# Kernel tuning notes

Measured on AMD Instinct MI355X. Metric: run time of the kernel, lower is better.

Reference implementation:

```python
import jax, jax.numpy as jnp
import numpy as np

N_NODES = 50000
N_EDGES = 1600000
N_FEAT = 128
DROPOUT = 0.1


def setup_inputs() -> dict:
    key = jax.random.key(0)
    k1, k2, k3, k4 = jax.random.split(key, 4)
    x = jax.random.normal(k1, (N_NODES, N_FEAT), dtype=jnp.float32)
    adj_vals = jax.random.uniform(k2, (N_EDGES,), dtype=jnp.float32)
    row = jax.random.randint(k3, (N_EDGES,), 0, N_NODES, dtype=jnp.int32)
    col = jax.random.randint(k4, (N_EDGES,), 0, N_NODES, dtype=jnp.int32)
    return {"x": x, "adj_vals": adj_vals, "row": row, "col": col}


def reference(x, adj_vals, row, col):
    # MixedDropout on sparse adjacency values (deterministic fixed key),
    # then SpMM: out[i] = sum_{e: row[e]==i} A_drop[e] * x[col[e]]
    keep_prob = 1.0 - DROPOUT
    mask_key = jax.random.fold_in(jax.random.key(42), 7)
    keep = jax.random.bernoulli(mask_key, keep_prob, adj_vals.shape)
    vals_drop = jnp.where(keep, adj_vals / keep_prob, 0.0)
    # gather source features and weight by (dropped) edge values
    msgs = vals_drop[:, None] * x[col]  # [E, F]
    out = jax.ops.segment_sum(msgs, row, num_segments=N_NODES)  # [N, F]
    return out
```

## Files before the change

### kernel.cpp

```cpp
#include <hip/hip_runtime.h>
#include <stdint.h>

#define N_NODES 50000
#define N_EDGES 1600000
#define N_FEAT 128
#define CAP 64
#define OVF_PW 256
#define OVF_PB 192

#define RSHIFT 8
#define BROWS 256
#define NB 196
#define NWG_A 250
#define A_THREADS 1024
#define CHUNKS_PW 1600
#define CAPW 56
#define NREG (NWG_A + NB)


struct KeyPair { uint32_t a, b; };

__host__ __device__ constexpr inline uint32_t rotl32(uint32_t x, int r) {
  return (x << r) | (x >> (32 - r));
}

__host__ __device__ constexpr inline KeyPair threefry2x32(uint32_t k0, uint32_t k1,
                                                          uint32_t x0, uint32_t x1) {
  const uint32_t ks0 = k0, ks1 = k1, ks2 = k0 ^ k1 ^ 0x1BD11BDAu;
  x0 += ks0;
  x1 += ks1;
  const int rotA[4] = {13, 15, 26, 6};
  const int rotB[4] = {17, 29, 16, 24};
  const uint32_t ks[3] = {ks0, ks1, ks2};
  for (int i = 0; i < 5; ++i) {
    const int* rot = (i & 1) ? rotB : rotA;
    for (int j = 0; j < 4; ++j) {
      x0 += x1;
      x1 = rotl32(x1, rot[j]);
      x1 ^= x0;
    }
    x0 += ks[(i + 1) % 3];
    x1 += ks[(i + 2) % 3] + (uint32_t)(i + 1);
  }
  return {x0, x1};
}

constexpr KeyPair MASK_KEY = threefry2x32(0u, 42u, 0u, 7u);

__device__ inline bool edge_keep(uint32_t e) {
  KeyPair r = threefry2x32(MASK_KEY.a, MASK_KEY.b, 0u, e);
  uint32_t bits = r.a ^ r.b;
  float u = __uint_as_float((bits >> 9) | 0x3f800000u) - 1.0f;
  return u < 0.9f;
}

__device__ inline uint32_t f2bf(uint32_t b) {
  return (b + 0x7fffu + ((b >> 16) & 1u)) >> 16;
}

typedef uint32_t u4v __attribute__((ext_vector_type(4)));
typedef float f4v __attribute__((ext_vector_type(4)));


__global__ void __launch_bounds__(A_THREADS) convA_kernel(const float* __restrict__ x,
                                                          uint32_t* __restrict__ xb,
                                                          const float* __restrict__ adj_vals,
                                                          const int* __restrict__ row,
                                                          const int* __restrict__ col,
                                                          uint64_t* __restrict__ coarse,
                                                          uint32_t* __restrict__ lens,
                                                          uint32_t* __restrict__ ovfcA,
                                                          uint64_t* __restrict__ ovfA) {
  __shared__ uint32_t cnt[NB];
  __shared__ uint32_t ovfc;
  int wg = blockIdx.x;
  int tid = threadIdx.x;
  if (tid < NB) cnt[tid] = 0;
  if (tid == 0) ovfc = 0;

  const int gthreads = NWG_A * A_THREADS;
  for (int i = wg * A_THREADS + tid; i < (N_NODES * N_FEAT) / 8; i += gthreads) {
    f4v a = ((const f4v*)x)[2 * i];
    f4v b = ((const f4v*)x)[2 * i + 1];
    u4v o;
    o.x = f2bf(__float_as_uint(a.x)) | (f2bf(__float_as_uint(a.y)) << 16);
    o.y = f2bf(__float_as_uint(a.z)) | (f2bf(__float_as_uint(a.w)) << 16);
    o.z = f2bf(__float_as_uint(b.x)) | (f2bf(__float_as_uint(b.y)) << 16);
    o.w = f2bf(__float_as_uint(b.z)) | (f2bf(__float_as_uint(b.w)) << 16);
    ((u4v*)xb)[i] = o;
  }
  __syncthreads();

  uint64_t* my_coarse = coarse + (size_t)wg * NB * CAPW;
  for (int ch = tid; ch < CHUNKS_PW; ch += A_THREADS) {
    const int g = wg * CHUNKS_PW + ch;
    const int4 r4 = ((const int4*)row)[g];
    const int4 c4 = ((const int4*)col)[g];
    const float4 a4 = ((const float4*)adj_vals)[g];
    const int rr[4] = {r4.x, r4.y, r4.z, r4.w};
    const int cc[4] = {c4.x, c4.y, c4.z, c4.w};
    const float aa[4] = {a4.x, a4.y, a4.z, a4.w};
#pragma unroll
    for (int k = 0; k < 4; ++k) {
      const uint32_t e = (uint32_t)(4 * g + k);
      if (!edge_keep(e)) continue;
      const uint32_t r = (uint32_t)rr[k];
      const uint32_t c = (uint32_t)cc[k];
      const float v = aa[k] / 0.9f;
      const uint32_t b = r >> RSHIFT;
      const uint32_t li = atomicAdd(&cnt[b], 1u);
      const uint64_t p = ((uint64_t)r << 48) | ((uint64_t)c << 32) | (uint64_t)__float_as_uint(v);
      if (li < CAPW) {
        my_coarse[(size_t)b * CAPW + li] = p;
      } else {
        const uint32_t oi = atomicAdd(&ovfc, 1u);
        if (oi < OVF_PW) ovfA[(size_t)wg * OVF_PW + oi] = p;
      }
    }
  }
  __syncthreads();
  if (tid < NB) lens[(size_t)tid * NWG_A + wg] = min(cnt[tid], (uint32_t)CAPW);
  if (tid == 0) ovfcA[wg] = min(ovfc, (uint32_t)OVF_PW);
}

__global__ void __launch_bounds__(1024) partB_kernel(const uint64_t* __restrict__ coarse,
                                                     const uint32_t* __restrict__ lens,
                                                     uint32_t* __restrict__ payload,
                                                     uint32_t* __restrict__ cursor,
                                                     uint32_t* __restrict__ ovfcB,
                                                     uint64_t* __restrict__ ovfB) {
  int b = blockIdx.x;
  int tid = threadIdx.x;
  __shared__ uint32_t cnt[BROWS];
  __shared__ uint32_t s_len[NWG_A];
  __shared__ uint32_t ovfc;
  if (tid < BROWS) cnt[tid] = 0;
  if (tid < NWG_A) s_len[tid] = lens[(size_t)b * NWG_A + tid];
  if (tid == 0) ovfc = 0;
  __syncthreads();

  int hw = tid >> 5;
  int lane = tid & 31;
  for (int seg = hw; seg < NWG_A; seg += 32) {
    uint32_t len = s_len[seg];
    const uint64_t* cseg = coarse + ((size_t)seg * NB + b) * CAPW;
    for (uint32_t li = (uint32_t)lane; li < len; li += 32) {
      uint64_t p = cseg[li];
      uint32_t r = (uint32_t)(p >> 48);
      uint32_t rl = r & (BROWS - 1);
      uint32_t idx = atomicAdd(&cnt[rl], 1u);
      if (idx < CAP) {
        uint32_t c = (uint32_t)(p >> 32) & 0xFFFFu;
        payload[(size_t)r * CAP + idx] = (c << 16) | f2bf((uint32_t)p);
      } else {
        uint32_t oi = atomicAdd(&ovfc, 1u);
        if (oi < OVF_PB) ovfB[(size_t)b * OVF_PB + oi] = p;
      }
    }
  }
  __syncthreads();
  if (tid < BROWS) {
    uint32_t r = ((uint32_t)b << RSHIFT) + (uint32_t)tid;
    if (r < N_NODES) {
      uint32_t c0 = min(cnt[tid], (uint32_t)CAP);
      cursor[r] = c0;
      uint32_t np = min((c0 + 7u) & ~7u, (uint32_t)CAP);
      for (uint32_t i2 = c0; i2 < np; ++i2) payload[(size_t)r * CAP + i2] = 0u;
    }
  }
  if (tid == 0) ovfcB[b] = min(ovfc, (uint32_t)OVF_PB);
}

__global__ void __launch_bounds__(256) gather_bf16_kernel(const uint32_t* __restrict__ xb,
                                                          const uint32_t* __restrict__ payload,
                                                          const uint32_t* __restrict__ cursor,
                                                          float* __restrict__ out) {
  int r = blockIdx.x * 16 + (threadIdx.x >> 4);
  int lane = threadIdx.x & 15;
  uint32_t base = (uint32_t)r * CAP;
  uint32_t cnt = cursor[r];
  uint32_t n = (cnt + 7u) & ~7u;
  const uint4* x4 = (const uint4*)xb;

  float acc0 = 0.f, acc1 = 0.f, acc2 = 0.f, acc3 = 0.f;
  float acc4 = 0.f, acc5 = 0.f, acc6 = 0.f, acc7 = 0.f;

  uint32_t p0 = __builtin_nontemporal_load(payload + base + lane);
  uint32_t p1 = __builtin_nontemporal_load(payload + base + 16 + lane);
  uint32_t p2 = (n > 32u) ? __builtin_nontemporal_load(payload + base + 32 + lane) : 0u;
  uint32_t p3 = (n > 48u) ? __builtin_nontemporal_load(payload + base + 48 + lane) : 0u;

#define GSTEP(ww)                                                            \
  {                                                                          \
    uint32_t cc = (ww) >> 16;                                                \
    float vv = __uint_as_float((ww) << 16);                                  \
    uint4 a = x4[(size_t)cc * 16 + lane];                                    \
    acc0 += vv * __uint_as_float(a.x << 16);                                 \
    acc1 += vv * __uint_as_float(a.x & 0xffff0000u);                         \
    acc2 += vv * __uint_as_float(a.y << 16);                                 \
    acc3 += vv * __uint_as_float(a.y & 0xffff0000u);                         \
    acc4 += vv * __uint_as_float(a.z << 16);                                 \
    acc5 += vv * __uint_as_float(a.z & 0xffff0000u);                         \
    acc6 += vv * __uint_as_float(a.w << 16);                                 \
    acc7 += vv * __uint_as_float(a.w & 0xffff0000u);                         \
  }

#define PCHUNK(preg, mm)                                                     \
  for (int j = 0; j < (mm); j += 8) {                                        \
    uint32_t w0 = __shfl((preg), j + 0, 16);                                 \
    uint32_t w1 = __shfl((preg), j + 1, 16);                                 \
    uint32_t w2 = __shfl((preg), j + 2, 16);                                 \
    uint32_t w3 = __shfl((preg), j + 3, 16);                                 \
    uint32_t w4 = __shfl((preg), j + 4, 16);                                 \
    uint32_t w5 = __shfl((preg), j + 5, 16);                                 \
    uint32_t w6 = __shfl((preg), j + 6, 16);                                 \
    uint32_t w7 = __shfl((preg), j + 7, 16);                                 \
    GSTEP(w0) GSTEP(w1) GSTEP(w2) GSTEP(w3)                                  \
    GSTEP(w4) GSTEP(w5) GSTEP(w6) GSTEP(w7)                                  \
  }

  int rem = (int)n;
  PCHUNK(p0, min(rem, 16));
  rem -= 16;
  if (rem > 0) {
    PCHUNK(p1, min(rem, 16));
    rem -= 16;
    if (rem > 0) {
      PCHUNK(p2, min(rem, 16));
      rem -= 16;
      if (rem > 0) {
        PCHUNK(p3, min(rem, 16));
      }
    }
  }
#undef PCHUNK
#undef GSTEP

  f4v lo, hi;
  lo.x = acc0; lo.y = acc1; lo.z = acc2; lo.w = acc3;
  hi.x = acc4; hi.y = acc5; hi.z = acc6; hi.w = acc7;
  f4v* o = (f4v*)out + (size_t)r * 32 + lane * 2;
  __builtin_nontemporal_store(lo, o);
  __builtin_nontemporal_store(hi, o + 1);
}

__global__ void __launch_bounds__(256) ovf_pack_kernel(const float* __restrict__ x,
                                                       const uint32_t* __restrict__ ovfcA,
                                                       const uint64_t* __restrict__ ovfA,
                                                       const uint32_t* __restrict__ ovfcB,
                                                       const uint64_t* __restrict__ ovfB,
                                                       float* __restrict__ out) {
  __shared__ int any;
  if (threadIdx.x == 0) any = 0;
  __syncthreads();
  for (int t = threadIdx.x; t < NREG; t += 256) {
    uint32_t c = (t < NWG_A) ? ovfcA[t] : ovfcB[t - NWG_A];
    if (c) any = 1;
  }
  __syncthreads();
  if (!any) return;

  int group = (int)((blockIdx.x * 256 + threadIdx.x) >> 7);
  int f = threadIdx.x & 127;
  const int ngroups = (16 * 256) >> 7;
  for (int reg = group; reg < NREG; reg += ngroups) {
    uint32_t c;
    const uint64_t* basep;
    if (reg < NWG_A) {
      c = min(ovfcA[reg], (uint32_t)OVF_PW);
      basep = ovfA + (size_t)reg * OVF_PW;
    } else {
      c = min(ovfcB[reg - NWG_A], (uint32_t)OVF_PB);
      basep = ovfB + (size_t)(reg - NWG_A) * OVF_PB;
    }
    for (uint32_t i = 0; i < c; ++i) {
      uint64_t p = basep[i];
      uint32_t r = (uint32_t)(p >> 48);
      uint32_t cc = (uint32_t)((p >> 32) & 0xFFFFu);
      float v = __uint_as_float((uint32_t)p);
      atomicAdd(&out[(size_t)r * N_FEAT + f], v * x[(size_t)cc * N_FEAT + f]);
    }
  }
}


__global__ void __launch_bounds__(256) scatter_fused_kernel(const float* __restrict__ x,
                                                            const float* __restrict__ adj_vals,
                                                            const int* __restrict__ row,
                                                            const int* __restrict__ col,
                                                            float* __restrict__ out) {
  long long t = (long long)blockIdx.x * blockDim.x + threadIdx.x;
  int e = (int)(t >> 6);
  int lane = (int)(t & 63);
  if (e >= N_EDGES) return;
  if (!edge_keep((uint32_t)e)) return;
  float v = adj_vals[e] / 0.9f;
  float2 xf = *(const float2*)(x + (long long)col[e] * N_FEAT + lane * 2);
  float* dst = out + (long long)row[e] * N_FEAT + lane * 2;
  atomicAdd(dst, v * xf.x);
  atomicAdd(dst + 1, v * xf.y);
}


extern "C" void kernel_launch(void* const* d_in, const int* in_sizes, int n_in,
                              void* d_out, int out_size, void* d_ws, size_t ws_size,
                              hipStream_t stream) {
  const float* x        = (const float*)d_in[0];
  const float* adj_vals = (const float*)d_in[1];
  const int*   row      = (const int*)d_in[2];
  const int*   col      = (const int*)d_in[3];
  float* out = (float*)d_out;

  size_t a_cursor  = 0;
  size_t a_ovfcA   = (a_cursor + (size_t)N_NODES * 4 + 255) & ~255ull;
  size_t a_ovfcB   = (a_ovfcA + (size_t)NWG_A * 4 + 255) & ~255ull;
  size_t a_lens    = (a_ovfcB + (size_t)NB * 4 + 255) & ~255ull;
  size_t a_ovfA    = (a_lens + (size_t)NB * NWG_A * 4 + 255) & ~255ull;
  size_t a_ovfB    = (a_ovfA + (size_t)NWG_A * OVF_PW * 8 + 255) & ~255ull;
  size_t a_coarse  = (a_ovfB + (size_t)NB * OVF_PB * 8 + 255) & ~255ull;
  size_t a_payload = (a_coarse + (size_t)NWG_A * NB * CAPW * 8 + 255) & ~255ull;
  size_t a_xb      = (a_payload + (size_t)N_NODES * CAP * 4 + 255) & ~255ull;
  size_t need      = a_xb + (size_t)N_NODES * N_FEAT * 2;

  if (ws_size >= need) {
    uint32_t* cursor  = (uint32_t*)((char*)d_ws + a_cursor);
    uint32_t* ovfcA   = (uint32_t*)((char*)d_ws + a_ovfcA);
    uint32_t* ovfcB   = (uint32_t*)((char*)d_ws + a_ovfcB);
    uint32_t* lens    = (uint32_t*)((char*)d_ws + a_lens);
    uint64_t* ovfA    = (uint64_t*)((char*)d_ws + a_ovfA);
    uint64_t* ovfB    = (uint64_t*)((char*)d_ws + a_ovfB);
    uint64_t* coarse  = (uint64_t*)((char*)d_ws + a_coarse);
    uint32_t* payload = (uint32_t*)((char*)d_ws + a_payload);
    uint32_t* xb      = (uint32_t*)((char*)d_ws + a_xb);

    convA_kernel<<<NWG_A, A_THREADS, 0, stream>>>(x, xb, adj_vals, row, col,
                                                  coarse, lens, ovfcA, ovfA);
    partB_kernel<<<NB, 1024, 0, stream>>>(coarse, lens, payload, cursor, ovfcB, ovfB);
    gather_bf16_kernel<<<N_NODES / 16, 256, 0, stream>>>(xb, payload, cursor, out);
    ovf_pack_kernel<<<16, 256, 0, stream>>>(x, ovfcA, ovfA, ovfcB, ovfB, out);
  } else {
    hipMemsetAsync(d_out, 0, (size_t)out_size * sizeof(float), stream);
    long long total_threads = (long long)N_EDGES * 64;
    scatter_fused_kernel<<<(int)((total_threads + 255) / 256), 256, 0, stream>>>(
        x, adj_vals, row, col, out);
  }
}
```

Baseline: 163.4 us.

## Fuse bucket ranking and bf16 gather into one kernel using LDS payload

Merges the second-level bucketing pass and the per-row gather into a single kernel. Each block ranks its edges into a shared-memory payload buffer, then gathers x rows and writes the output directly. This removes the global payload and cursor round trip and one kernel launch. To fit in LDS, the bucket size is halved to 128 rows, the block count is doubled, and the per-workgroup capacity is reduced, which may raise overflow frequency and cut gather parallelism to 391 blocks of 512 threads.

```diff
diff --git a/kernel.cpp b/kernel.cpp
--- a/kernel.cpp
+++ b/kernel.cpp
@@ -8,13 +8,13 @@
 #define OVF_PW 256
 #define OVF_PB 192
 
-#define RSHIFT 8
-#define BROWS 256
-#define NB 196
+#define RSHIFT 7
+#define BROWS 128
+#define NB 391
 #define NWG_A 250
 #define A_THREADS 1024
 #define CHUNKS_PW 1600
-#define CAPW 56
+#define CAPW 40
 #define NREG (NWG_A + NB)
 
 
@@ -123,35 +123,38 @@
   if (tid == 0) ovfcA[wg] = min(ovfc, (uint32_t)OVF_PW);
 }
 
-__global__ void __launch_bounds__(1024) partB_kernel(const uint64_t* __restrict__ coarse,
-                                                     const uint32_t* __restrict__ lens,
-                                                     uint32_t* __restrict__ payload,
-                                                     uint32_t* __restrict__ cursor,
-                                                     uint32_t* __restrict__ ovfcB,
-                                                     uint64_t* __restrict__ ovfB) {
+__global__ void __launch_bounds__(512) rank_gather_kernel(const uint32_t* __restrict__ xb,
+                                                          const uint64_t* __restrict__ coarse,
+                                                          const uint32_t* __restrict__ lens,
+                                                          uint32_t* __restrict__ ovfcB,
+                                                          uint64_t* __restrict__ ovfB,
+                                                          float* __restrict__ out) {
   int b = blockIdx.x;
   int tid = threadIdx.x;
+  __shared__ uint32_t pay[BROWS * CAP];
   __shared__ uint32_t cnt[BROWS];
   __shared__ uint32_t s_len[NWG_A];
   __shared__ uint32_t ovfc;
+  for (int i = tid; i < BROWS * CAP; i += 512) pay[i] = 0u;
   if (tid < BROWS) cnt[tid] = 0;
   if (tid < NWG_A) s_len[tid] = lens[(size_t)b * NWG_A + tid];
   if (tid == 0) ovfc = 0;
   __syncthreads();
 
-  int hw = tid >> 5;
-  int lane = tid & 31;
-  for (int seg = hw; seg < NWG_A; seg += 32) {
+  int team = tid >> 4;
+  int lane = tid & 15;
+
+  for (int seg = team; seg < NWG_A; seg += 32) {
     uint32_t len = s_len[seg];
     const uint64_t* cseg = coarse + ((size_t)seg * NB + b) * CAPW;
-    for (uint32_t li = (uint32_t)lane; li < len; li += 32) {
-      uint64_t p = cseg[li];
+    for (uint32_t li = (uint32_t)lane; li < len; li += 16) {
+      uint64_t p = __builtin_nontemporal_load(cseg + li);
       uint32_t r = (uint32_t)(p >> 48);
       uint32_t rl = r & (BROWS - 1);
       uint32_t idx = atomicAdd(&cnt[rl], 1u);
       if (idx < CAP) {
         uint32_t c = (uint32_t)(p >> 32) & 0xFFFFu;
-        payload[(size_t)r * CAP + idx] = (c << 16) | f2bf((uint32_t)p);
+        pay[rl * CAP + idx] = (c << 16) | f2bf((uint32_t)p);
       } else {
         uint32_t oi = atomicAdd(&ovfc, 1u);
         if (oi < OVF_PB) ovfB[(size_t)b * OVF_PB + oi] = p;
@@ -159,36 +162,10 @@
     }
   }
   __syncthreads();
-  if (tid < BROWS) {
-    uint32_t r = ((uint32_t)b << RSHIFT) + (uint32_t)tid;
-    if (r < N_NODES) {
-      uint32_t c0 = min(cnt[tid], (uint32_t)CAP);
-      cursor[r] = c0;
-      uint32_t np = min((c0 + 7u) & ~7u, (uint32_t)CAP);
-      for (uint32_t i2 = c0; i2 < np; ++i2) payload[(size_t)r * CAP + i2] = 0u;
-    }
-  }
   if (tid == 0) ovfcB[b] = min(ovfc, (uint32_t)OVF_PB);
-}
-
-__global__ void __launch_bounds__(256) gather_bf16_kernel(const uint32_t* __restrict__ xb,
-                                                          const uint32_t* __restrict__ payload,
-                                                          const uint32_t* __restrict__ cursor,
-                                                          float* __restrict__ out) {
-  int r = blockIdx.x * 16 + (threadIdx.x >> 4);
-  int lane = threadIdx.x & 15;
-  uint32_t base = (uint32_t)r * CAP;
-  uint32_t cnt = cursor[r];
-  uint32_t n = (cnt + 7u) & ~7u;
+
   const uint4* x4 = (const uint4*)xb;
-
-  float acc0 = 0.f, acc1 = 0.f, acc2 = 0.f, acc3 = 0.f;
-  float acc4 = 0.f, acc5 = 0.f, acc6 = 0.f, acc7 = 0.f;
-
-  uint32_t p0 = __builtin_nontemporal_load(payload + base + lane);
-  uint32_t p1 = __builtin_nontemporal_load(payload + base + 16 + lane);
-  uint32_t p2 = (n > 32u) ? __builtin_nontemporal_load(payload + base + 32 + lane) : 0u;
-  uint32_t p3 = (n > 48u) ? __builtin_nontemporal_load(payload + base + 48 + lane) : 0u;
+  const int r0 = b << RSHIFT;
 
 #define GSTEP(ww)                                                            \
   {                                                                          \
@@ -205,43 +182,33 @@
     acc7 += vv * __uint_as_float(a.w & 0xffff0000u);                         \
   }
 
-#define PCHUNK(preg, mm)                                                     \
-  for (int j = 0; j < (mm); j += 8) {                                        \
-    uint32_t w0 = __shfl((preg), j + 0, 16);                                 \
-    uint32_t w1 = __shfl((preg), j + 1, 16);                                 \
-    uint32_t w2 = __shfl((preg), j + 2, 16);                                 \
-    uint32_t w3 = __shfl((preg), j + 3, 16);                                 \
-    uint32_t w4 = __shfl((preg), j + 4, 16);                                 \
-    uint32_t w5 = __shfl((preg), j + 5, 16);                                 \
-    uint32_t w6 = __shfl((preg), j + 6, 16);                                 \
-    uint32_t w7 = __shfl((preg), j + 7, 16);                                 \
-    GSTEP(w0) GSTEP(w1) GSTEP(w2) GSTEP(w3)                                  \
-    GSTEP(w4) GSTEP(w5) GSTEP(w6) GSTEP(w7)                                  \
-  }
-
-  int rem = (int)n;
-  PCHUNK(p0, min(rem, 16));
-  rem -= 16;
-  if (rem > 0) {
-    PCHUNK(p1, min(rem, 16));
-    rem -= 16;
-    if (rem > 0) {
-      PCHUNK(p2, min(rem, 16));
-      rem -= 16;
-      if (rem > 0) {
-        PCHUNK(p3, min(rem, 16));
-      }
-    }
-  }
-#undef PCHUNK
+  for (int rl = team; rl < BROWS; rl += 32) {
+    int r = r0 + rl;
+    if (r >= N_NODES) continue;
+    uint32_t n = (min(cnt[rl], (uint32_t)CAP) + 7u) & ~7u;
+    const uint32_t* prow = &pay[rl * CAP];
+    float acc0 = 0.f, acc1 = 0.f, acc2 = 0.f, acc3 = 0.f;
+    float acc4 = 0.f, acc5 = 0.f, acc6 = 0.f, acc7 = 0.f;
+    for (uint32_t j = 0; j < n; j += 8) {
+      uint32_t w0 = prow[j + 0];
+      uint32_t w1 = prow[j + 1];
+      uint32_t w2 = prow[j + 2];
+      uint32_t w3 = prow[j + 3];
+      uint32_t w4 = prow[j + 4];
+      uint32_t w5 = prow[j + 5];
+      uint32_t w6 = prow[j + 6];
+      uint32_t w7 = prow[j + 7];
+      GSTEP(w0) GSTEP(w1) GSTEP(w2) GSTEP(w3)
+      GSTEP(w4) GSTEP(w5) GSTEP(w6) GSTEP(w7)
+    }
+    f4v lo, hi;
+    lo.x = acc0; lo.y = acc1; lo.z = acc2; lo.w = acc3;
+    hi.x = acc4; hi.y = acc5; hi.z = acc6; hi.w = acc7;
+    f4v* o = (f4v*)out + (size_t)r * 32 + lane * 2;
+    __builtin_nontemporal_store(lo, o);
+    __builtin_nontemporal_store(hi, o + 1);
+  }
 #undef GSTEP
-
-  f4v lo, hi;
-  lo.x = acc0; lo.y = acc1; lo.z = acc2; lo.w = acc3;
-  hi.x = acc4; hi.y = acc5; hi.z = acc6; hi.w = acc7;
-  f4v* o = (f4v*)out + (size_t)r * 32 + lane * 2;
-  __builtin_nontemporal_store(lo, o);
-  __builtin_nontemporal_store(hi, o + 1);
 }
 
 __global__ void __launch_bounds__(256) ovf_pack_kernel(const float* __restrict__ x,
@@ -311,32 +278,27 @@
   const int*   col      = (const int*)d_in[3];
   float* out = (float*)d_out;
 
-  size_t a_cursor  = 0;
-  size_t a_ovfcA   = (a_cursor + (size_t)N_NODES * 4 + 255) & ~255ull;
+  size_t a_ovfcA   = 0;
   size_t a_ovfcB   = (a_ovfcA + (size_t)NWG_A * 4 + 255) & ~255ull;
   size_t a_lens    = (a_ovfcB + (size_t)NB * 4 + 255) & ~255ull;
   size_t a_ovfA    = (a_lens + (size_t)NB * NWG_A * 4 + 255) & ~255ull;
   size_t a_ovfB    = (a_ovfA + (size_t)NWG_A * OVF_PW * 8 + 255) & ~255ull;
   size_t a_coarse  = (a_ovfB + (size_t)NB * OVF_PB * 8 + 255) & ~255ull;
-  size_t a_payload = (a_coarse + (size_t)NWG_A * NB * CAPW * 8 + 255) & ~255ull;
-  size_t a_xb      = (a_payload + (size_t)N_NODES * CAP * 4 + 255) & ~255ull;
+  size_t a_xb      = (a_coarse + (size_t)NWG_A * NB * CAPW * 8 + 255) & ~255ull;
   size_t need      = a_xb + (size_t)N_NODES * N_FEAT * 2;
 
   if (ws_size >= need) {
-    uint32_t* cursor  = (uint32_t*)((char*)d_ws + a_cursor);
     uint32_t* ovfcA   = (uint32_t*)((char*)d_ws + a_ovfcA);
     uint32_t* ovfcB   = (uint32_t*)((char*)d_ws + a_ovfcB);
     uint32_t* lens    = (uint32_t*)((char*)d_ws + a_lens);
     uint64_t* ovfA    = (uint64_t*)((char*)d_ws + a_ovfA);
     uint64_t* ovfB    = (uint64_t*)((char*)d_ws + a_ovfB);
     uint64_t* coarse  = (uint64_t*)((char*)d_ws + a_coarse);
-    uint32_t* payload = (uint32_t*)((char*)d_ws + a_payload);
     uint32_t* xb      = (uint32_t*)((char*)d_ws + a_xb);
 
     convA_kernel<<<NWG_A, A_THREADS, 0, stream>>>(x, xb, adj_vals, row, col,
                                                   coarse, lens, ovfcA, ovfA);
-    partB_kernel<<<NB, 1024, 0, stream>>>(coarse, lens, payload, cursor, ovfcB, ovfB);
-    gather_bf16_kernel<<<N_NODES / 16, 256, 0, stream>>>(xb, payload, cursor, out);
+    rank_gather_kernel<<<NB, 512, 0, stream>>>(xb, coarse, lens, ovfcB, ovfB, out);
     ovf_pack_kernel<<<16, 256, 0, stream>>>(x, ovfcA, ovfA, ovfcB, ovfB, out);
   } else {
     hipMemsetAsync(d_out, 0, (size_t)out_size * sizeof(float), stream);
```

Result: faster. 155.1 us (-5.1%).
